# Kernel tuning notes

Measured on AMD Instinct MI355X. Metric: run time of the kernel, lower is better.

## Reference

```python
import jax, jax.numpy as jnp
import numpy as np

B, L, DC, DQ, H = 32, 1024, 1024, 1024, 512
NEG_NUM = -10000.0


def setup_inputs() -> dict:
    key = jax.random.key(0)
    ks = jax.random.split(key, 7)
    s1 = 1.0 / np.sqrt(DC + DQ)
    s2 = 1.0 / np.sqrt(H)
    return {
        "ctx": jax.random.normal(ks[0], (B, L, DC), jnp.float32),
        "query": jax.random.normal(ks[1], (B, DQ), jnp.float32),
        "mask": jnp.ones((B, L), jnp.int32),
        "noise": jax.random.normal(ks[2], (B, L), jnp.float32),
        "W1": jax.random.uniform(ks[3], (DC + DQ, H), jnp.float32, -s1, s1),
        "b1": jax.random.uniform(ks[4], (H,), jnp.float32, -s1, s1),
        "w2": jax.random.uniform(ks[5], (H,), jnp.float32, -s2, s2),
        "b2": jnp.zeros((), jnp.float32),
    }


def reference(ctx, query, mask, noise, W1, b1, w2, b2):
    b, l, dc = ctx.shape
    # concat([ctx, query_expanded]) @ W1 == ctx @ W1[:DC] + query @ W1[DC:]
    hidden = jnp.tanh(
        jnp.einsum("blc,ch->blh", ctx, W1[:dc])
        + (query @ W1[dc:])[:, None, :]
        + b1
    )  # [B, L, H]
    score = hidden @ w2 + b2  # [B, L]
    score = jnp.where(mask == 0, NEG_NUM, score)
    score = score + noise  # sigmoid_noise=True -> coefficient 1
    p = jax.nn.sigmoid(score)  # p_choose_i [B, L]

    # initial prev_att: one-hot at position 0
    prev_att = jnp.zeros((b, l), score.dtype).at[:, 0].set(1.0)
    # shifted (1 - p): [1, 1-p_0, ..., 1-p_{L-2}]
    shifted = jnp.concatenate(
        [jnp.ones((b, 1), p.dtype), 1.0 - p[:, :-1]], axis=1
    )

    # linear recurrence a_t = shifted_t * a_{t-1} + prev_att_t  (a_{-1}=0)
    def step(carry, xs):
        s_t, pr_t = xs
        a = s_t * carry + pr_t
        return a, a

    _, att_t = jax.lax.scan(step, jnp.zeros((b,), p.dtype), (shifted.T, prev_att.T))
    att = att_t.T * p  # [B, L]

    expected_ctx = jnp.einsum("bl,blc->bc", att, ctx)  # bmm(p_ctx[:,None,:], ctx)
    return expected_ctx, att
```

## Files before the change

kernel.cpp:

```cpp
#include <hip/hip_runtime.h>
#include <hip/hip_bf16.h>
#include <math.h>

constexpr int Bb = 32;
constexpr int Ll = 1024;
constexpr int DC = 1024;
constexpr int DQ = 1024;
constexpr int Hh = 512;
#define NEG_NUM -10000.0f

typedef __attribute__((ext_vector_type(8))) short bf16x8;
typedef __attribute__((ext_vector_type(4))) float f32x4;

#define GLOAD_LDS16(g, l)                                                  \
    __builtin_amdgcn_global_load_lds(                                      \
        (const __attribute__((address_space(1))) void*)(g),                \
        (__attribute__((address_space(3))) void*)(l), 16, 0, 0)

__device__ inline unsigned short f2bf(float f) {
    unsigned int x = __float_as_uint(f);
    unsigned int r = (x + 0x7FFFu + ((x >> 16) & 1u)) >> 16;
    return (unsigned short)r;
}
__device__ inline float bfu(unsigned short u) {
    return __uint_as_float(((unsigned int)u) << 16);
}


__global__ __launch_bounds__(256) void prep_kernel(const float* __restrict__ W1,
                                                   const float* __restrict__ query,
                                                   const float* __restrict__ b1,
                                                   const float* __restrict__ ctx,
                                                   unsigned short* __restrict__ w1t,
                                                   float* __restrict__ qb,
                                                   float* __restrict__ score,
                                                   float* __restrict__ out_ctx,
                                                   unsigned short* __restrict__ ctxb) {
    __shared__ float red[4][64];
    const int bid = blockIdx.x;
    if (bid < 2048) {
        int idx = bid * 256 + threadIdx.x;
        int n = idx >> 10, k = idx & 1023;
        int ks = k ^ ((n & 7) << 3);
        w1t[(size_t)n * 1024 + ks] = f2bf(W1[(size_t)k * Hh + n]);
    } else if (bid < 2176) {
        int i = (bid - 2048) * 256 + threadIdx.x;
        out_ctx[i] = 0.f;
        score[i] = 0.f;
    } else if (bid < 2432) {
        const int qbid = bid - 2176;
        const int b  = qbid >> 3;
        const int hg = qbid & 7;
        const int hl = threadIdx.x & 63;
        const int j  = threadIdx.x >> 6;
        const int h  = hg * 64 + hl;
        const float* q = query + (size_t)b * DQ + j * 256;
        const float* w = W1 + (size_t)(DC + j * 256) * Hh + h;
        float a0 = 0.f, a1 = 0.f, a2 = 0.f, a3 = 0.f;
#pragma unroll 4
        for (int c = 0; c < 256; c += 4) {
            a0 += q[c + 0] * w[(size_t)(c + 0) * Hh];
            a1 += q[c + 1] * w[(size_t)(c + 1) * Hh];
            a2 += q[c + 2] * w[(size_t)(c + 2) * Hh];
            a3 += q[c + 3] * w[(size_t)(c + 3) * Hh];
        }
        red[j][hl] = (a0 + a1) + (a2 + a3);
        __syncthreads();
        if (j == 0)
            qb[(size_t)b * Hh + h] = red[0][hl] + red[1][hl] + red[2][hl] + red[3][hl] + b1[h];
    } else {
        size_t i = (size_t)((bid - 2432) * 256 + threadIdx.x) * 8;
        int row = (int)(i >> 10);
        int col = (int)(i & 1023);
        float4 v0 = *(const float4*)(ctx + i);
        float4 v1 = *(const float4*)(ctx + i + 4);
        union { unsigned short us[8]; uint4 v; } o;
        o.us[0] = f2bf(v0.x); o.us[1] = f2bf(v0.y); o.us[2] = f2bf(v0.z); o.us[3] = f2bf(v0.w);
        o.us[4] = f2bf(v1.x); o.us[5] = f2bf(v1.y); o.us[6] = f2bf(v1.z); o.us[7] = f2bf(v1.w);
        *(uint4*)(ctxb + ((size_t)row << 10) + (col ^ ((row & 7) << 3))) = o.v;
    }
}

__global__ __launch_bounds__(512, 1) void gemm_mfma(const unsigned short* __restrict__ ctxb,
                                                    const unsigned short* __restrict__ w1t,
                                                    const float* __restrict__ qb,
                                                    const float* __restrict__ w2,
                                                    float* __restrict__ score) {
    __shared__ unsigned short lds[2 * 32768];

    const int bid = blockIdx.x;
    const int n0 = ((bid >> 3) & 1) * 256;
    const int m0 = (((bid >> 4) << 3) | (bid & 7)) * 256;

    const int tid = threadIdx.x;
    const int wv = tid >> 6, lane = tid & 63;
    const int wr = wv >> 2, wc = wv & 3;
    const int lr = lane & 15, lk = lane >> 4;

    char* ldsB = (char*)lds;
    const char* ctxB = (const char*)ctxb;
    const char* w1tB = (const char*)w1t;

    const int srow = tid >> 3;
    const int scolb = (tid & 7) * 16;
    const int x = (lr & 7) << 4;

    f32x4 acc[8][4];
#pragma unroll
    for (int mf = 0; mf < 8; ++mf)
#pragma unroll
        for (int nf = 0; nf < 4; ++nf) acc[mf][nf] = (f32x4){0.f, 0.f, 0.f, 0.f};

#pragma unroll
    for (int i = 0; i < 4; ++i) {
        int row = i * 64 + srow;
        GLOAD_LDS16(ctxB + (size_t)(m0 + row) * 2048 + scolb,
                    ldsB + i * 8192 + tid * 16);
        GLOAD_LDS16(w1tB + (size_t)(n0 + row) * 2048 + scolb,
                    ldsB + 32768 + i * 8192 + tid * 16);
    }

    for (int ks = 0; ks < 16; ++ks) {
        const int cur = ks & 1;
        char* bufc = ldsB + cur * 65536;

        __builtin_amdgcn_s_barrier();
        if (ks < 15) {
            char* bufn = ldsB + (cur ^ 1) * 65536;
            const int kb = (ks + 1) * 128;
#pragma unroll
            for (int i = 0; i < 4; ++i) {
                int row = i * 64 + srow;
                GLOAD_LDS16(ctxB + (size_t)(m0 + row) * 2048 + kb + scolb,
                            bufn + i * 8192 + tid * 16);
                GLOAD_LDS16(w1tB + (size_t)(n0 + row) * 2048 + kb + scolb,
                            bufn + 32768 + i * 8192 + tid * 16);
            }
            asm volatile("s_waitcnt vmcnt(8)" ::: "memory");
        } else {
            asm volatile("s_waitcnt vmcnt(0)" ::: "memory");
        }
        __builtin_amdgcn_sched_barrier(0);
        __builtin_amdgcn_s_barrier();

#pragma unroll
        for (int kk = 0; kk < 2; ++kk) {
            const int colb = (kk * 64 + lk * 16) ^ x;
            bf16x8 a[8], bb[4];
#pragma unroll
            for (int nf = 0; nf < 4; ++nf)
                bb[nf] = *(const bf16x8*)(bufc + 32768 + (wc * 64 + nf * 16 + lr) * 128 + colb);
#pragma unroll
            for (int mf = 0; mf < 8; ++mf)
                a[mf] = *(const bf16x8*)(bufc + (wr * 128 + mf * 16 + lr) * 128 + colb);
#pragma unroll
            for (int mf = 0; mf < 8; ++mf)
#pragma unroll
                for (int nf = 0; nf < 4; ++nf)
                    acc[mf][nf] = __builtin_amdgcn_mfma_f32_16x16x32_bf16(a[mf], bb[nf], acc[mf][nf], 0, 0, 0);
        }
    }

    const int bq = m0 >> 10;
    const float* qbb = qb + (size_t)bq * Hh;
#pragma unroll
    for (int mf = 0; mf < 8; ++mf) {
        float s0 = 0.f, s1 = 0.f, s2 = 0.f, s3 = 0.f;
#pragma unroll
        for (int nf = 0; nf < 4; ++nf) {
            int col = n0 + wc * 64 + nf * 16 + lr;
            float wvw = w2[col];
            float qv = qbb[col];
            s0 += tanhf(acc[mf][nf][0] + qv) * wvw;
            s1 += tanhf(acc[mf][nf][1] + qv) * wvw;
            s2 += tanhf(acc[mf][nf][2] + qv) * wvw;
            s3 += tanhf(acc[mf][nf][3] + qv) * wvw;
        }
#pragma unroll
        for (int off = 8; off; off >>= 1) {
            s0 += __shfl_xor(s0, off, 16);
            s1 += __shfl_xor(s1, off, 16);
            s2 += __shfl_xor(s2, off, 16);
            s3 += __shfl_xor(s3, off, 16);
        }
        if (lr == 0) {
            int row = m0 + wr * 128 + mf * 16 + lk * 4;
            atomicAdd(&score[row + 0], s0);
            atomicAdd(&score[row + 1], s1);
            atomicAdd(&score[row + 2], s2);
            atomicAdd(&score[row + 3], s3);
        }
    }
}

__global__ __launch_bounds__(64) void scan_kernel(const float* __restrict__ score,
                                                  const int* __restrict__ mask,
                                                  const float* __restrict__ noise,
                                                  const float* __restrict__ b2p,
                                                  float* __restrict__ att) {
    int b = blockIdx.x;
    int lane = threadIdx.x;
    float b2 = b2p[0];
    int base = b * Ll + lane * 16;

    float p[16], q[16];
    float run = 1.f;
#pragma unroll
    for (int j = 0; j < 16; ++j) {
        int l = base + j;
        float s = score[l] + b2;
        if (mask[l] == 0) s = NEG_NUM;
        s += noise[l];
        float pv = 1.f / (1.f + expf(-s));
        p[j] = pv;
        run *= (1.f - pv);
        q[j] = run;
    }
    float incl = run;
#pragma unroll
    for (int off = 1; off < 64; off <<= 1) {
        float v = __shfl_up(incl, off, 64);
        if (lane >= off) incl *= v;
    }
    float excl = __shfl_up(incl, 1, 64);
    if (lane == 0) excl = 1.f;
#pragma unroll
    for (int j = 0; j < 16; ++j) {
        float P = excl * (j == 0 ? 1.f : q[j - 1]);
        att[base + j] = p[j] * P;
    }
}

__global__ __launch_bounds__(256) void ectx_bf16_kernel(const unsigned short* __restrict__ ctxb,
                                                        const float* __restrict__ att,
                                                        float* __restrict__ out) {
    int b = blockIdx.z;
    int c4 = threadIdx.x;
    int l0 = blockIdx.y * 128;
    const unsigned short* cb = ctxb + ((size_t)b * Ll + l0) * DC;
    const float* ab = att + (size_t)b * Ll + l0;
    const int c = c4 * 4;
    float a0 = 0.f, a1 = 0.f, a2 = 0.f, a3 = 0.f;
    for (int l = 0; l < 128; ++l) {
        float av = ab[l];
        int cs = c ^ ((l & 7) << 3);
        ushort4 v = *(const ushort4*)(cb + (size_t)l * DC + cs);
        a0 += av * bfu(v.x); a1 += av * bfu(v.y);
        a2 += av * bfu(v.z); a3 += av * bfu(v.w);
    }
    float* o = out + (size_t)b * DC + c;
    atomicAdd(o + 0, a0); atomicAdd(o + 1, a1);
    atomicAdd(o + 2, a2); atomicAdd(o + 3, a3);
}

extern "C" void kernel_launch(void* const* d_in, const int* in_sizes, int n_in,
                              void* d_out, int out_size, void* d_ws, size_t ws_size,
                              hipStream_t stream) {
    const float* ctx   = (const float*)d_in[0];
    const float* query = (const float*)d_in[1];
    const int*   mask  = (const int*)d_in[2];
    const float* noise = (const float*)d_in[3];
    const float* W1    = (const float*)d_in[4];
    const float* b1    = (const float*)d_in[5];
    const float* w2    = (const float*)d_in[6];
    const float* b2    = (const float*)d_in[7];

    float* out_ctx = (float*)d_out;
    float* out_att = (float*)d_out + Bb * DC;

    char* ws = (char*)d_ws;
    float* score = (float*)ws;
    float* qb    = (float*)(ws + 131072);
    unsigned short* w1t  = (unsigned short*)(ws + 196608);
    unsigned short* ctxb = (unsigned short*)(ws + 1245184);

    prep_kernel<<<18816, 256, 0, stream>>>(W1, query, b1, ctx, w1t, qb, score, out_ctx, ctxb);

    gemm_mfma<<<256, 512, 0, stream>>>(ctxb, w1t, qb, w2, score);

    scan_kernel<<<Bb, 64, 0, stream>>>(score, mask, noise, b2, out_att);

    ectx_bf16_kernel<<<dim3(1, Ll / 128, Bb), 256, 0, stream>>>(ctxb, out_att, out_ctx);
}
```

Before: 99.44 us.

## Split GEMM prefetch across k-halves, raise MFMA priority, fuse scan into ectx

In the GEMM main loop, the next-tile global-to-LDS prefetch is split into two halves. The second half is issued after the first MFMA sub-step, and MFMA blocks are wrapped in s_setprio to favour matrix issue. The separate scan kernel is folded into the expected-context kernel: each block recomputes the whole-row sigmoid and prefix product into shared memory, and one block per batch writes att. This removes a launch and the att round-trip, at the cost of redundant scan work in 8 blocks per batch and an extra barrier per k-step in the GEMM.

```diff
diff --git a/kernel.cpp b/kernel.cpp
--- a/kernel.cpp
+++ b/kernel.cpp
@@ -123,29 +123,28 @@
     for (int ks = 0; ks < 16; ++ks) {
         const int cur = ks & 1;
         char* bufc = ldsB + cur * 65536;
+        char* bufn = ldsB + (cur ^ 1) * 65536;
+        const int kb = (ks + 1) * 128;
 
         __builtin_amdgcn_s_barrier();
         if (ks < 15) {
-            char* bufn = ldsB + (cur ^ 1) * 65536;
-            const int kb = (ks + 1) * 128;
-#pragma unroll
-            for (int i = 0; i < 4; ++i) {
+#pragma unroll
+            for (int i = 0; i < 2; ++i) {
                 int row = i * 64 + srow;
                 GLOAD_LDS16(ctxB + (size_t)(m0 + row) * 2048 + kb + scolb,
                             bufn + i * 8192 + tid * 16);
                 GLOAD_LDS16(w1tB + (size_t)(n0 + row) * 2048 + kb + scolb,
                             bufn + 32768 + i * 8192 + tid * 16);
             }
-            asm volatile("s_waitcnt vmcnt(8)" ::: "memory");
+            asm volatile("s_waitcnt vmcnt(4)" ::: "memory");
         } else {
             asm volatile("s_waitcnt vmcnt(0)" ::: "memory");
         }
         __builtin_amdgcn_sched_barrier(0);
         __builtin_amdgcn_s_barrier();
 
-#pragma unroll
-        for (int kk = 0; kk < 2; ++kk) {
-            const int colb = (kk * 64 + lk * 16) ^ x;
+        {
+            const int colb = (lk * 16) ^ x;
             bf16x8 a[8], bb[4];
 #pragma unroll
             for (int nf = 0; nf < 4; ++nf)
@@ -153,11 +152,41 @@
 #pragma unroll
             for (int mf = 0; mf < 8; ++mf)
                 a[mf] = *(const bf16x8*)(bufc + (wr * 128 + mf * 16 + lr) * 128 + colb);
+            __builtin_amdgcn_s_setprio(1);
 #pragma unroll
             for (int mf = 0; mf < 8; ++mf)
 #pragma unroll
                 for (int nf = 0; nf < 4; ++nf)
                     acc[mf][nf] = __builtin_amdgcn_mfma_f32_16x16x32_bf16(a[mf], bb[nf], acc[mf][nf], 0, 0, 0);
+            __builtin_amdgcn_s_setprio(0);
+        }
+        __builtin_amdgcn_s_barrier();
+        if (ks < 15) {
+#pragma unroll
+            for (int i = 2; i < 4; ++i) {
+                int row = i * 64 + srow;
+                GLOAD_LDS16(ctxB + (size_t)(m0 + row) * 2048 + kb + scolb,
+                            bufn + i * 8192 + tid * 16);
+                GLOAD_LDS16(w1tB + (size_t)(n0 + row) * 2048 + kb + scolb,
+                            bufn + 32768 + i * 8192 + tid * 16);
+            }
+        }
+        {
+            const int colb = (64 + lk * 16) ^ x;
+            bf16x8 a[8], bb[4];
+#pragma unroll
+            for (int nf = 0; nf < 4; ++nf)
+                bb[nf] = *(const bf16x8*)(bufc + 32768 + (wc * 64 + nf * 16 + lr) * 128 + colb);
+#pragma unroll
+            for (int mf = 0; mf < 8; ++mf)
+                a[mf] = *(const bf16x8*)(bufc + (wr * 128 + mf * 16 + lr) * 128 + colb);
+            __builtin_amdgcn_s_setprio(1);
+#pragma unroll
+            for (int mf = 0; mf < 8; ++mf)
+#pragma unroll
+                for (int nf = 0; nf < 4; ++nf)
+                    acc[mf][nf] = __builtin_amdgcn_mfma_f32_16x16x32_bf16(a[mf], bb[nf], acc[mf][nf], 0, 0, 0);
+            __builtin_amdgcn_s_setprio(0);
         }
     }
 
@@ -193,56 +222,59 @@
     }
 }
 
-__global__ __launch_bounds__(64) void scan_kernel(const float* __restrict__ score,
+__global__ __launch_bounds__(256) void ectx_fused(const unsigned short* __restrict__ ctxb,
+                                                  const float* __restrict__ score,
                                                   const int* __restrict__ mask,
                                                   const float* __restrict__ noise,
                                                   const float* __restrict__ b2p,
-                                                  float* __restrict__ att) {
-    int b = blockIdx.x;
-    int lane = threadIdx.x;
-    float b2 = b2p[0];
-    int base = b * Ll + lane * 16;
-
-    float p[16], q[16];
-    float run = 1.f;
-#pragma unroll
-    for (int j = 0; j < 16; ++j) {
-        int l = base + j;
-        float s = score[l] + b2;
-        if (mask[l] == 0) s = NEG_NUM;
-        s += noise[l];
-        float pv = 1.f / (1.f + expf(-s));
-        p[j] = pv;
-        run *= (1.f - pv);
-        q[j] = run;
-    }
-    float incl = run;
-#pragma unroll
-    for (int off = 1; off < 64; off <<= 1) {
-        float v = __shfl_up(incl, off, 64);
-        if (lane >= off) incl *= v;
-    }
-    float excl = __shfl_up(incl, 1, 64);
-    if (lane == 0) excl = 1.f;
-#pragma unroll
-    for (int j = 0; j < 16; ++j) {
-        float P = excl * (j == 0 ? 1.f : q[j - 1]);
-        att[base + j] = p[j] * P;
-    }
-}
-
-__global__ __launch_bounds__(256) void ectx_bf16_kernel(const unsigned short* __restrict__ ctxb,
-                                                        const float* __restrict__ att,
-                                                        float* __restrict__ out) {
-    int b = blockIdx.z;
-    int c4 = threadIdx.x;
-    int l0 = blockIdx.y * 128;
+                                                  float* __restrict__ att_out,
+                                                  float* __restrict__ out) {
+    __shared__ float att_s[1024];
+    const int b = blockIdx.z;
+    const int ly = blockIdx.y;
+    const int tid = threadIdx.x;
+
+    if (tid < 64) {
+        const int lane = tid;
+        const float b2 = b2p[0];
+        const int base = b * Ll + lane * 16;
+        float p[16], q[16];
+        float run = 1.f;
+#pragma unroll
+        for (int j = 0; j < 16; ++j) {
+            int l = base + j;
+            float s = score[l] + b2;
+            if (mask[l] == 0) s = NEG_NUM;
+            s += noise[l];
+            float pv = 1.f / (1.f + expf(-s));
+            p[j] = pv;
+            run *= (1.f - pv);
+            q[j] = run;
+        }
+        float incl = run;
+#pragma unroll
+        for (int off = 1; off < 64; off <<= 1) {
+            float v = __shfl_up(incl, off, 64);
+            if (lane >= off) incl *= v;
+        }
+        float excl = __shfl_up(incl, 1, 64);
+        if (lane == 0) excl = 1.f;
+#pragma unroll
+        for (int j = 0; j < 16; ++j) {
+            float P = excl * (j == 0 ? 1.f : q[j - 1]);
+            float av = p[j] * P;
+            att_s[lane * 16 + j] = av;
+            if (ly == 0) att_out[base + j] = av;
+        }
+    }
+    __syncthreads();
+
+    const int l0 = ly * 128;
     const unsigned short* cb = ctxb + ((size_t)b * Ll + l0) * DC;
-    const float* ab = att + (size_t)b * Ll + l0;
-    const int c = c4 * 4;
+    const int c = tid * 4;
     float a0 = 0.f, a1 = 0.f, a2 = 0.f, a3 = 0.f;
     for (int l = 0; l < 128; ++l) {
-        float av = ab[l];
+        float av = att_s[l0 + l];
         int cs = c ^ ((l & 7) << 3);
         ushort4 v = *(const ushort4*)(cb + (size_t)l * DC + cs);
         a0 += av * bfu(v.x); a1 += av * bfu(v.y);
@@ -278,7 +310,6 @@
 
     gemm_mfma<<<256, 512, 0, stream>>>(ctxb, w1t, qb, w2, score);
 
-    scan_kernel<<<Bb, 64, 0, stream>>>(score, mask, noise, b2, out_att);
-
-    ectx_bf16_kernel<<<dim3(1, Ll / 128, Bb), 256, 0, stream>>>(ctxb, out_att, out_ctx);
-}
+    ectx_fused<<<dim3(1, Ll / 128, Bb), 256, 0, stream>>>(ctxb, score, mask, noise, b2,
+                                                          out_att, out_ctx);
+}
```

After: 101.3 us. No clear change (+1.9%).
